# Kernel tuning notes

Hardware: AMD Instinct MI355X
Metric: run time of the kernel (lower is better)

## Reference

```python
import jax, jax.numpy as jnp
import numpy as np
from jax import lax

NUM_BLOCKS = 3
NUM_LAYERS = 10
NL = NUM_BLOCKS * NUM_LAYERS  # 30 res blocks
RC = 512   # residual channels
GC = 512   # gate channels
SC = 512   # skip channels
KS = 2     # kernel size
CIN = 128  # local-conditioning channels
FRONT = 32 # front conv kernel size
OUT = 2    # gaussian (mean, log_std)
UPS = [16, 16]  # upsample scales, product = 256 hop
SQRT_HALF = 0.7071067811865476


def causal_conv1d(x, w, b, dilation):
    # x: [B,C_in,T], w: [C_out,C_in,K] -> left-pad only == torch pad-both + trim right (causal SAME)
    pad = dilation * (w.shape[-1] - 1)
    y = lax.conv_general_dilated(x, w, window_strides=(1,), padding=[(pad, 0)],
                                 rhs_dilation=(dilation,),
                                 dimension_numbers=('NCH', 'OIH', 'NCH'))
    return y + b[None, :, None]


def pw(x, w, b):
    # 1x1 conv: w [C_out,C_in]
    return jnp.einsum('oi,bit->bot', w, x) + b[None, :, None]


def upsample(c, up_w, up_b):
    # c: [B,CIN,Tm]; torch ConvTranspose2d(1,1,(3,2s),pad=(1,s//2),stride=(1,s)) + LeakyReLU(0.4)
    h = c[:, None]  # [B,1,CIN,Tm]
    for j, s in enumerate(UPS):
        k = up_w[j][:, :, ::-1, ::-1]  # flip kernel: transposed conv as lhs-dilated conv
        pw_ = 2 * s - 1 - s // 2       # = K - 1 - torch_pad along width
        h = lax.conv_general_dilated(h, k, window_strides=(1, 1),
                                     padding=[(1, 1), (pw_, pw_)],
                                     lhs_dilation=(1, s),
                                     dimension_numbers=('NCHW', 'OIHW', 'NCHW')) + up_b[j]
        h = jnp.where(h > 0, h, 0.4 * h)  # LeakyReLU(0.4)
    return h[:, 0]  # [B,CIN,T]


def setup_inputs() -> dict:
    key = jax.random.key(0)
    ks = iter(jax.random.split(key, 32))
    def rn(shape, scale):
        return jax.random.normal(next(ks), shape, dtype=jnp.float32) * scale
    B, T_mel = 1, 16
    T = T_mel * 256
    return {
        'x': rn((B, 1, T), 1.0),
        'c': rn((B, CIN, T_mel), 1.0),
        'front_w': rn((RC, 1, FRONT), 0.2),
        'front_b': rn((RC,), 0.05),
        'filt_w': rn((NL, GC, RC, KS), 0.03),
        'filt_b': rn((NL, GC), 0.05),
        'gate_w': rn((NL, GC, RC, KS), 0.03),
        'gate_b': rn((NL, GC), 0.05),
        'cf_w': rn((NL, GC, CIN), 0.05),
        'cf_b': rn((NL, GC), 0.05),
        'cg_w': rn((NL, GC, CIN), 0.05),
        'cg_b': rn((NL, GC), 0.05),
        'res_w': rn((NL, RC, GC), 0.04),
        'res_b': rn((NL, RC), 0.05),
        'skip_w': rn((NL, SC, GC), 0.04),
        'skip_b': rn((NL, SC), 0.05),
        'fin1_w': rn((SC, SC), 0.04),
        'fin1_b': rn((SC,), 0.05),
        'fin2_w': rn((OUT, SC), 0.04),
        'fin2_b': rn((OUT,), 0.05),
        'up_w': rn((2, 1, 1, 3, 2 * 16), 0.1),
        'up_b': rn((2,), 0.05),
    }


def reference(x, c, front_w, front_b, filt_w, filt_b, gate_w, gate_b,
              cf_w, cf_b, cg_w, cg_b, res_w, res_b, skip_w, skip_b,
              fin1_w, fin1_b, fin2_w, fin2_b, up_w, up_b):
    c_up = upsample(c, up_w, up_b)                       # [B,CIN,T]
    h = jax.nn.relu(causal_conv1d(x, front_w, front_b, 1))  # [B,RC,T]
    skip = jnp.zeros((x.shape[0], SC, x.shape[2]), x.dtype)
    for i in range(NL):
        d = KS ** (i % NUM_LAYERS)
        f = causal_conv1d(h, filt_w[i], filt_b[i], d) + pw(c_up, cf_w[i], cf_b[i])
        g = causal_conv1d(h, gate_w[i], gate_b[i], d) + pw(c_up, cg_w[i], cg_b[i])
        o = jnp.tanh(f) * jax.nn.sigmoid(g)
        h = (h + pw(o, res_w[i], res_b[i])) * SQRT_HALF
        skip = skip + pw(o, skip_w[i], skip_b[i])
    out = jax.nn.relu(skip)
    out = jax.nn.relu(pw(out, fin1_w, fin1_b))
    return pw(out, fin2_w, fin2_b)  # [B,OUT,T]
```

## Files before the change

### kernel.cpp

```cpp
#include <hip/hip_runtime.h>
#include <hip/hip_bf16.h>

#define TLEN 4096
#define HPADT 512
#define SQRT_HALF 0.70710678118654752f

typedef __attribute__((ext_vector_type(8))) short short8;
typedef __attribute__((ext_vector_type(4))) float floatx4;
typedef __attribute__((ext_vector_type(4))) unsigned short ushort4v;

#define MFMA_BF16(a, b, c) __builtin_amdgcn_mfma_f32_16x16x32_bf16((a), (b), (c), 0, 0, 0)

__device__ __forceinline__ float bf2f(unsigned short u) {
  union { unsigned int i; float f; } v; v.i = ((unsigned int)u) << 16; return v.f;
}
__device__ __forceinline__ unsigned short f2bf(float x) {
  union { float f; unsigned int i; } v; v.f = x;
  unsigned int r = v.i + 0x7FFFu + ((v.i >> 16) & 1u);
  return (unsigned short)(r >> 16);
}
__device__ __forceinline__ short8 ld8(const unsigned short* p) { return *(const short8*)p; }

template <int NI>
__device__ __forceinline__ void stage128(unsigned short* lds, const unsigned short* src,
                                         int stride, int tid) {
  #pragma unroll
  for (int inst = 0; inst < NI; ++inst) {
    int qb = inst * 256 + (tid & 192);
    int q = qb + (tid & 63);
    int r = q >> 4;
    int c = (q & 15) ^ (r & 15);
    __builtin_amdgcn_global_load_lds(
        (const __attribute__((address_space(1))) unsigned int*)(src + (size_t)r * stride + (c << 3)),
        (__attribute__((address_space(3))) unsigned int*)(lds + qb * 8),
        16, 0, 0);
  }
}

__device__ __forceinline__ short8 frag128(const unsigned short* lds, int r, int cj) {
  return *(const short8*)(lds + r * 128 + ((cj ^ (r & 15)) << 3));
}

__global__ __launch_bounds__(256) void cast_all_kernel(
    const float* __restrict__ fw, const float* __restrict__ gw,
    const float* __restrict__ rw, const float* __restrict__ sw,
    const float* __restrict__ cf, const float* __restrict__ cg,
    const float* __restrict__ f1, const float* __restrict__ fb,
    const float* __restrict__ cfb, const float* __restrict__ gb,
    const float* __restrict__ cgb,
    unsigned short* __restrict__ WA, unsigned short* __restrict__ RS,
    unsigned short* __restrict__ CA, unsigned short* __restrict__ F1c,
    float* __restrict__ fgb)
{
  int b = blockIdx.x;
  if (b < 7680) {
    size_t idx = (size_t)b * 256 + threadIdx.x;
    size_t l = idx >> 16;
    int o = (int)((idx >> 7) & 511);
    int i4 = (int)(idx & 127) * 4;
    const float4* fp = (const float4*)(fw + (((l * 512 + o) * 512 + i4) * 2));
    const float4* gp = (const float4*)(gw + (((l * 512 + o) * 512 + i4) * 2));
    float4 f0 = fp[0], f1v = fp[1];
    float4 g0 = gp[0], g1 = gp[1];
    size_t base0 = ((l * 2 + 0) * 1024);
    size_t base1 = ((l * 2 + 1) * 1024);
    *(ushort4v*)&WA[(base0 + o) * 512 + i4]       = (ushort4v){f2bf(f0.x), f2bf(f0.z), f2bf(f1v.x), f2bf(f1v.z)};
    *(ushort4v*)&WA[(base1 + o) * 512 + i4]       = (ushort4v){f2bf(f0.y), f2bf(f0.w), f2bf(f1v.y), f2bf(f1v.w)};
    *(ushort4v*)&WA[(base0 + 512 + o) * 512 + i4] = (ushort4v){f2bf(g0.x), f2bf(g0.z), f2bf(g1.x), f2bf(g1.z)};
    *(ushort4v*)&WA[(base1 + 512 + o) * 512 + i4] = (ushort4v){f2bf(g0.y), f2bf(g0.w), f2bf(g1.y), f2bf(g1.w)};
  } else if (b < 15360) {
    size_t idx = (size_t)(b - 7680) * 256 + threadIdx.x;
    size_t l = idx >> 16;
    int o = (int)((idx >> 7) & 511);
    int i4 = (int)(idx & 127) * 4;
    float4 r4 = *(const float4*)(rw + ((l * 512 + o) * 512 + i4));
    float4 s4 = *(const float4*)(sw + ((l * 512 + o) * 512 + i4));
    *(ushort4v*)&RS[(l * 1024 + o) * 512 + i4]       = (ushort4v){f2bf(r4.x), f2bf(r4.y), f2bf(r4.z), f2bf(r4.w)};
    *(ushort4v*)&RS[(l * 1024 + 512 + o) * 512 + i4] = (ushort4v){f2bf(s4.x), f2bf(s4.y), f2bf(s4.z), f2bf(s4.w)};
  } else if (b < 17280) {
    size_t idx = (size_t)(b - 15360) * 256 + threadIdx.x;
    size_t l = idx >> 14;
    int o = (int)((idx >> 5) & 511);
    int i4 = (int)(idx & 31) * 4;
    float4 f4 = *(const float4*)(cf + ((l * 512 + o) * 128 + i4));
    float4 g4 = *(const float4*)(cg + ((l * 512 + o) * 128 + i4));
    *(ushort4v*)&CA[(l * 1024 + o) * 128 + i4]       = (ushort4v){f2bf(f4.x), f2bf(f4.y), f2bf(f4.z), f2bf(f4.w)};
    *(ushort4v*)&CA[(l * 1024 + 512 + o) * 128 + i4] = (ushort4v){f2bf(g4.x), f2bf(g4.y), f2bf(g4.z), f2bf(g4.w)};
  } else if (b < 17536) {
    size_t idx = (size_t)(b - 17280) * 256 + threadIdx.x;
    float4 v = *(const float4*)(f1 + idx * 4);
    *(ushort4v*)&F1c[idx * 4] = (ushort4v){f2bf(v.x), f2bf(v.y), f2bf(v.z), f2bf(v.w)};
  } else {
    int idx = (b - 17536) * 256 + threadIdx.x;
    int l = idx >> 10, r = idx & 1023;
    float v;
    if (r < 512) v = fb[l * 512 + r] + cfb[l * 512 + r];
    else         v = gb[l * 512 + r - 512] + cgb[l * 512 + r - 512];
    fgb[idx] = v;
  }
}


__global__ __launch_bounds__(256) void upsample1_kernel(
    const float* __restrict__ c, const float* __restrict__ up_w,
    const float* __restrict__ up_b, float* __restrict__ u1)
{
  int x = threadIdx.x;
  int h = blockIdx.x;
  const float* w = up_w;
  float acc = 0.f;
  int k1 = (23 - x) & 15;
  #pragma unroll
  for (int dk = 0; dk < 2; ++dk) {
    int kx = k1 + 16 * dk;
    int num = x + kx - 23;
    if (num >= 0) {
      int qq = num >> 4;
      if (qq < 16) {
        #pragma unroll
        for (int ky = 0; ky < 3; ++ky) {
          int hh = h + ky - 1;
          if (hh >= 0 && hh < 128)
            acc += c[hh * 16 + qq] * w[(2 - ky) * 32 + (31 - kx)];
        }
      }
    }
  }
  acc += up_b[0];
  u1[h * 256 + x] = acc > 0.f ? acc : 0.4f * acc;
}

__global__ __launch_bounds__(256) void upsample2_kernel(
    const float* __restrict__ u1, const float* __restrict__ up_w,
    const float* __restrict__ up_b, unsigned short* __restrict__ cu)
{
  int x = blockIdx.x * 256 + threadIdx.x;
  int h = blockIdx.y;
  const float* w = up_w + 96;
  float acc = 0.f;
  int k1 = (23 - x) & 15;
  #pragma unroll
  for (int dk = 0; dk < 2; ++dk) {
    int kx = k1 + 16 * dk;
    int num = x + kx - 23;
    if (num >= 0) {
      int qq = num >> 4;
      if (qq < 256) {
        #pragma unroll
        for (int ky = 0; ky < 3; ++ky) {
          int hh = h + ky - 1;
          if (hh >= 0 && hh < 128)
            acc += u1[hh * 256 + qq] * w[(2 - ky) * 32 + (31 - kx)];
        }
      }
    }
  }
  acc += up_b[1];
  acc = acc > 0.f ? acc : 0.4f * acc;
  cu[(size_t)x * 128 + h] = f2bf(acc);
}

__global__ __launch_bounds__(256) void front_kernel(
    const float* __restrict__ x, const float* __restrict__ fw, const float* __restrict__ fb,
    float* __restrict__ hf, unsigned short* __restrict__ hbf)
{
  __shared__ float xs[40];
  int tid = threadIdx.x;
  int o = blockIdx.y * 256 + tid;
  int t0 = blockIdx.x * 8;
  if (tid < 39) {
    int gx = t0 - 31 + tid;
    xs[tid] = (gx >= 0) ? x[gx] : 0.f;
  }
  __syncthreads();
  float w[32];
  #pragma unroll
  for (int k = 0; k < 32; ++k) w[k] = fw[o * 32 + k];
  float b = fb[o];
  #pragma unroll
  for (int j = 0; j < 8; ++j) {
    float acc = b;
    #pragma unroll
    for (int k = 0; k < 32; ++k) acc += w[k] * xs[j + k];
    acc = acc > 0.f ? acc : 0.f;
    int t = t0 + j;
    hf[(size_t)t * 512 + o] = acc;
    hbf[(size_t)(HPADT + t) * 512 + o] = f2bf(acc);
  }
}

__global__ __launch_bounds__(256) void gemm_a_kernel(
    const unsigned short* __restrict__ WA,
    const unsigned short* __restrict__ CA,
    const float* __restrict__ fgb,
    const unsigned short* __restrict__ hbf,
    const unsigned short* __restrict__ cu,
    unsigned short* __restrict__ obf,
    const int d)
{
  __shared__ unsigned short Af[2][64 * 128];
  __shared__ unsigned short Ag[2][64 * 128];
  __shared__ unsigned short Xs[2][128 * 128];

  const int tid = threadIdx.x;
  const int lane = tid & 63;
  const int wave = tid >> 6;
  const int lm = lane & 15, qd = lane >> 4;
  const int n0 = blockIdx.x * 128;
  const int m0 = blockIdx.y * 64;
  const int wm = (wave & 1) * 32;
  const int wn = (wave >> 1) * 64;

  floatx4 accF[2][4], accG[2][4];
  #pragma unroll
  for (int a = 0; a < 2; ++a)
    #pragma unroll
    for (int b = 0; b < 4; ++b) {
      accF[a][b] = (floatx4){0.f, 0.f, 0.f, 0.f};
      accG[a][b] = (floatx4){0.f, 0.f, 0.f, 0.f};
    }

  auto stage_step = [&](int s, int b) {
    if (s < 8) {
      int tap = s >> 2;
      int k0 = (s & 3) * 128;
      const unsigned short* ab = WA + (size_t)tap * 524288;
      stage128<4>(&Af[b][0], ab + (size_t)m0 * 512 + k0, 512, tid);
      stage128<4>(&Ag[b][0], ab + (size_t)(512 + m0) * 512 + k0, 512, tid);
      stage128<8>(&Xs[b][0], hbf + (size_t)(HPADT + n0 - (tap ? 0 : d)) * 512 + k0, 512, tid);
    } else {
      stage128<4>(&Af[b][0], CA + (size_t)m0 * 128, 128, tid);
      stage128<4>(&Ag[b][0], CA + (size_t)(512 + m0) * 128, 128, tid);
      stage128<8>(&Xs[b][0], cu + (size_t)n0 * 128, 128, tid);
    }
  };

  stage_step(0, 0);
  for (int s = 0; s < 9; ++s) {
    __syncthreads();
    if (s < 8) stage_step(s + 1, (s + 1) & 1);
    const unsigned short* af = &Af[s & 1][0];
    const unsigned short* ag = &Ag[s & 1][0];
    const unsigned short* xs = &Xs[s & 1][0];
    #pragma unroll
    for (int j = 0; j < 4; ++j) {
      int cj = j * 4 + qd;
      short8 a[2], g[2], xv[4];
      a[0] = frag128(af, wm + lm, cj);
      a[1] = frag128(af, wm + 16 + lm, cj);
      g[0] = frag128(ag, wm + lm, cj);
      g[1] = frag128(ag, wm + 16 + lm, cj);
      #pragma unroll
      for (int nt = 0; nt < 4; ++nt) xv[nt] = frag128(xs, wn + nt * 16 + lm, cj);
      #pragma unroll
      for (int mt = 0; mt < 2; ++mt)
        #pragma unroll
        for (int nt = 0; nt < 4; ++nt) {
          accF[mt][nt] = MFMA_BF16(a[mt], xv[nt], accF[mt][nt]);
          accG[mt][nt] = MFMA_BF16(g[mt], xv[nt], accG[mt][nt]);
        }
    }
  }

  #pragma unroll
  for (int mt = 0; mt < 2; ++mt) {
    int oc0 = m0 + wm + mt * 16 + qd * 4;
    floatx4 fb4 = *(const floatx4*)&fgb[oc0];
    floatx4 gb4 = *(const floatx4*)&fgb[512 + oc0];
    #pragma unroll
    for (int nt = 0; nt < 4; ++nt) {
      int t = n0 + wn + nt * 16 + lm;
      ushort4v o4;
      #pragma unroll
      for (int r = 0; r < 4; ++r) {
        float f = accF[mt][nt][r] + fb4[r];
        float g = accG[mt][nt][r] + gb4[r];
        float ef = __expf(-2.f * f);
        float th = (1.f - ef) / (1.f + ef);
        float sg = 1.f / (1.f + __expf(-g));
        o4[r] = f2bf(th * sg);
      }
      *(ushort4v*)&obf[(size_t)t * 512 + oc0] = o4;
    }
  }
}

__global__ __launch_bounds__(256) void gemm_b_kernel(
    const unsigned short* __restrict__ RS,
    const float* __restrict__ rb, const float* __restrict__ sb,
    const unsigned short* __restrict__ obf,
    float* __restrict__ hf, unsigned short* __restrict__ hbf,
    float* __restrict__ skip, unsigned short* __restrict__ skipbf,
    const int first, const int last)
{
  __shared__ unsigned short Ar[2][64 * 128];
  __shared__ unsigned short As_[2][64 * 128];
  __shared__ unsigned short Xs[2][128 * 128];

  const int tid = threadIdx.x;
  const int lane = tid & 63;
  const int wave = tid >> 6;
  const int lm = lane & 15, qd = lane >> 4;
  const int n0 = blockIdx.x * 128;
  const int m0 = blockIdx.y * 64;
  const int wm = (wave & 1) * 32;
  const int wn = (wave >> 1) * 64;

  floatx4 accR[2][4], accS[2][4];
  #pragma unroll
  for (int a = 0; a < 2; ++a)
    #pragma unroll
    for (int b = 0; b < 4; ++b) {
      accR[a][b] = (floatx4){0.f, 0.f, 0.f, 0.f};
      accS[a][b] = (floatx4){0.f, 0.f, 0.f, 0.f};
    }

  auto stage_step = [&](int s, int b) {
    int k0 = s * 128;
    stage128<4>(&Ar[b][0], RS + (size_t)m0 * 512 + k0, 512, tid);
    stage128<4>(&As_[b][0], RS + (size_t)(512 + m0) * 512 + k0, 512, tid);
    stage128<8>(&Xs[b][0], obf + (size_t)n0 * 512 + k0, 512, tid);
  };

  stage_step(0, 0);
  for (int s = 0; s < 4; ++s) {
    __syncthreads();
    if (s < 3) stage_step(s + 1, (s + 1) & 1);
    const unsigned short* ar = &Ar[s & 1][0];
    const unsigned short* as = &As_[s & 1][0];
    const unsigned short* xs = &Xs[s & 1][0];
    #pragma unroll
    for (int j = 0; j < 4; ++j) {
      int cj = j * 4 + qd;
      short8 a[2], g[2], xv[4];
      a[0] = frag128(ar, wm + lm, cj);
      a[1] = frag128(ar, wm + 16 + lm, cj);
      g[0] = frag128(as, wm + lm, cj);
      g[1] = frag128(as, wm + 16 + lm, cj);
      #pragma unroll
      for (int nt = 0; nt < 4; ++nt) xv[nt] = frag128(xs, wn + nt * 16 + lm, cj);
      #pragma unroll
      for (int mt = 0; mt < 2; ++mt)
        #pragma unroll
        for (int nt = 0; nt < 4; ++nt) {
          accR[mt][nt] = MFMA_BF16(a[mt], xv[nt], accR[mt][nt]);
          accS[mt][nt] = MFMA_BF16(g[mt], xv[nt], accS[mt][nt]);
        }
    }
  }

  #pragma unroll
  for (int mt = 0; mt < 2; ++mt) {
    int oc0 = m0 + wm + mt * 16 + qd * 4;
    floatx4 rb4 = *(const floatx4*)&rb[oc0];
    floatx4 sb4 = *(const floatx4*)&sb[oc0];
    #pragma unroll
    for (int nt = 0; nt < 4; ++nt) {
      int t = n0 + wn + nt * 16 + lm;
      size_t base = (size_t)t * 512 + oc0;
      floatx4 h4 = *(const floatx4*)&hf[base];
      floatx4 s4;
      if (first) s4 = (floatx4){0.f, 0.f, 0.f, 0.f};
      else s4 = *(const floatx4*)&skip[base];
      ushort4v hb4;
      #pragma unroll
      for (int r = 0; r < 4; ++r) {
        float hv = (h4[r] + accR[mt][nt][r] + rb4[r]) * SQRT_HALF;
        h4[r] = hv;
        hb4[r] = f2bf(hv);
        s4[r] = s4[r] + accS[mt][nt][r] + sb4[r];
      }
      *(floatx4*)&hf[base] = h4;
      *(ushort4v*)&hbf[(size_t)(HPADT + t) * 512 + oc0] = hb4;
      *(floatx4*)&skip[base] = s4;
      if (last) {
        ushort4v sk4;
        #pragma unroll
        for (int r = 0; r < 4; ++r) sk4[r] = f2bf(s4[r] > 0.f ? s4[r] : 0.f);
        *(ushort4v*)&skipbf[base] = sk4;
      }
    }
  }
}

__global__ __launch_bounds__(256) void final1_kernel(
    const unsigned short* __restrict__ W1,
    const float* __restrict__ b1,
    const unsigned short* __restrict__ skipbf,
    unsigned short* __restrict__ t1)
{
  __shared__ unsigned short Aw[2][64 * 128];
  __shared__ unsigned short Xs[2][128 * 128];

  const int tid = threadIdx.x;
  const int lane = tid & 63;
  const int wave = tid >> 6;
  const int lm = lane & 15, qd = lane >> 4;
  const int n0 = blockIdx.x * 128;
  const int m0 = blockIdx.y * 64;
  const int wm = (wave & 1) * 32;
  const int wn = (wave >> 1) * 64;

  floatx4 acc[2][4];
  #pragma unroll
  for (int a = 0; a < 2; ++a)
    #pragma unroll
    for (int b = 0; b < 4; ++b) acc[a][b] = (floatx4){0.f, 0.f, 0.f, 0.f};

  auto stage_step = [&](int s, int b) {
    int k0 = s * 128;
    stage128<4>(&Aw[b][0], W1 + (size_t)m0 * 512 + k0, 512, tid);
    stage128<8>(&Xs[b][0], skipbf + (size_t)n0 * 512 + k0, 512, tid);
  };

  stage_step(0, 0);
  for (int s = 0; s < 4; ++s) {
    __syncthreads();
    if (s < 3) stage_step(s + 1, (s + 1) & 1);
    const unsigned short* aw = &Aw[s & 1][0];
    const unsigned short* xs = &Xs[s & 1][0];
    #pragma unroll
    for (int j = 0; j < 4; ++j) {
      int cj = j * 4 + qd;
      short8 a[2], xv[4];
      a[0] = frag128(aw, wm + lm, cj);
      a[1] = frag128(aw, wm + 16 + lm, cj);
      #pragma unroll
      for (int nt = 0; nt < 4; ++nt) xv[nt] = frag128(xs, wn + nt * 16 + lm, cj);
      #pragma unroll
      for (int mt = 0; mt < 2; ++mt)
        #pragma unroll
        for (int nt = 0; nt < 4; ++nt)
          acc[mt][nt] = MFMA_BF16(a[mt], xv[nt], acc[mt][nt]);
    }
  }

  #pragma unroll
  for (int mt = 0; mt < 2; ++mt) {
    int oc0 = m0 + wm + mt * 16 + qd * 4;
    floatx4 b4 = *(const floatx4*)&b1[oc0];
    #pragma unroll
    for (int nt = 0; nt < 4; ++nt) {
      int t = n0 + wn + nt * 16 + lm;
      ushort4v o4;
      #pragma unroll
      for (int r = 0; r < 4; ++r) {
        float v = acc[mt][nt][r] + b4[r];
        o4[r] = f2bf(v > 0.f ? v : 0.f);
      }
      *(ushort4v*)&t1[(size_t)t * 512 + oc0] = o4;
    }
  }
}

__global__ __launch_bounds__(256) void final2_kernel(
    const float* __restrict__ W2, const float* __restrict__ b2,
    const unsigned short* __restrict__ t1, float* __restrict__ out)
{
  int wave = threadIdx.x >> 6, lane = threadIdx.x & 63;
  int t = blockIdx.x * 4 + wave;
  short8 v = ld8(t1 + (size_t)t * 512 + lane * 8);
  float a0 = 0.f, a1 = 0.f;
  #pragma unroll
  for (int r = 0; r < 8; ++r) {
    float f = bf2f((unsigned short)v[r]);
    a0 += W2[lane * 8 + r] * f;
    a1 += W2[512 + lane * 8 + r] * f;
  }
  #pragma unroll
  for (int off = 32; off > 0; off >>= 1) {
    a0 += __shfl_xor(a0, off, 64);
    a1 += __shfl_xor(a1, off, 64);
  }
  if (lane == 0) {
    out[t] = a0 + b2[0];
    out[TLEN + t] = a1 + b2[1];
  }
}

extern "C" void kernel_launch(void* const* d_in, const int* in_sizes, int n_in,
                              void* d_out, int out_size, void* d_ws, size_t ws_size,
                              hipStream_t stream) {
  (void)in_sizes; (void)n_in; (void)out_size; (void)ws_size;
  const float* x       = (const float*)d_in[0];
  const float* c       = (const float*)d_in[1];
  const float* front_w = (const float*)d_in[2];
  const float* front_b = (const float*)d_in[3];
  const float* filt_w  = (const float*)d_in[4];
  const float* filt_b  = (const float*)d_in[5];
  const float* gate_w  = (const float*)d_in[6];
  const float* gate_b  = (const float*)d_in[7];
  const float* cf_w    = (const float*)d_in[8];
  const float* cf_b    = (const float*)d_in[9];
  const float* cg_w    = (const float*)d_in[10];
  const float* cg_b    = (const float*)d_in[11];
  const float* res_w   = (const float*)d_in[12];
  const float* res_b   = (const float*)d_in[13];
  const float* skip_w  = (const float*)d_in[14];
  const float* skip_b  = (const float*)d_in[15];
  const float* fin1_w  = (const float*)d_in[16];
  const float* fin1_b  = (const float*)d_in[17];
  const float* fin2_w  = (const float*)d_in[18];
  const float* fin2_b  = (const float*)d_in[19];
  const float* up_w    = (const float*)d_in[20];
  const float* up_b    = (const float*)d_in[21];

  char* ws = (char*)d_ws;
  auto alloc = [&](size_t bytes) {
    char* p = ws;
    ws += (bytes + 255) & ~(size_t)255;
    return p;
  };
  unsigned short* WA     = (unsigned short*)alloc((size_t)30 * 2 * 1024 * 512 * 2);
  unsigned short* RS     = (unsigned short*)alloc((size_t)30 * 1024 * 512 * 2);
  unsigned short* CA     = (unsigned short*)alloc((size_t)30 * 1024 * 128 * 2);
  unsigned short* F1c    = (unsigned short*)alloc((size_t)512 * 512 * 2);
  float* fgb             = (float*)alloc((size_t)30 * 1024 * 4);
  float* u1              = (float*)alloc((size_t)128 * 256 * 4);
  unsigned short* cu     = (unsigned short*)alloc((size_t)TLEN * 128 * 2);
  float* hf              = (float*)alloc((size_t)TLEN * 512 * 4);
  unsigned short* hbf    = (unsigned short*)alloc((size_t)(HPADT + TLEN) * 512 * 2);
  unsigned short* obf    = (unsigned short*)alloc((size_t)TLEN * 512 * 2);
  float* skip            = (float*)alloc((size_t)TLEN * 512 * 4);
  unsigned short* skipbf = (unsigned short*)alloc((size_t)TLEN * 512 * 2);
  unsigned short* t1     = (unsigned short*)alloc((size_t)TLEN * 512 * 2);
  float* out             = (float*)d_out;

  hipMemsetAsync(hbf, 0, (size_t)HPADT * 512 * 2, stream);

  cast_all_kernel<<<17656, 256, 0, stream>>>(
      filt_w, gate_w, res_w, skip_w, cf_w, cg_w, fin1_w,
      filt_b, cf_b, gate_b, cg_b, WA, RS, CA, F1c, fgb);

  upsample1_kernel<<<dim3(128), 256, 0, stream>>>(c, up_w, up_b, u1);
  upsample2_kernel<<<dim3(16, 128), 256, 0, stream>>>(u1, up_w, up_b, cu);
  front_kernel<<<dim3(512, 2), 256, 0, stream>>>(x, front_w, front_b, hf, hbf);

  for (int l = 0; l < 30; ++l) {
    int d = 1 << (l % 10);
    gemm_a_kernel<<<dim3(32, 8), 256, 0, stream>>>(
        WA + (size_t)l * 2 * 524288, CA + (size_t)l * 131072,
        fgb + (size_t)l * 1024,
        hbf, cu, obf, d);
    gemm_b_kernel<<<dim3(32, 8), 256, 0, stream>>>(
        RS + (size_t)l * 524288,
        res_b + (size_t)l * 512, skip_b + (size_t)l * 512,
        obf, hf, hbf, skip, skipbf, (l == 0) ? 1 : 0, (l == 29) ? 1 : 0);
  }

  final1_kernel<<<dim3(32, 8), 256, 0, stream>>>(F1c, fin1_b, skipbf, t1);
  final2_kernel<<<1024, 256, 0, stream>>>(fin2_w, fin2_b, t1, out);
}
```

Measured before the change: 1.286 ms.

## Fuse 30-layer residual loop into one persistent kernel with grid barriers

Replaces the 60 per-layer gemm_a/gemm_b launches with a single persistent kernel of 256 blocks that loops over all layers and uses an atomic-counter grid barrier between phases. The fp32 residual state h and the skip accumulator are held in registers across layers, so the fp32 hf/skip global reads and writes disappear and the skip buffer is removed. This saves launch overhead and memory traffic, but it relies on all 256 blocks being co-resident and adds spin-wait barrier cost. The barrier's bounded spin guard could also silently break correctness if a wait times out.

Measured after the change: 1.864 ms. 1.45x slower.

```diff
diff --git a/kernel.cpp b/kernel.cpp
--- a/kernel.cpp
+++ b/kernel.cpp
@@ -39,6 +39,19 @@
 
 __device__ __forceinline__ short8 frag128(const unsigned short* lds, int r, int cj) {
   return *(const short8*)(lds + r * 128 + ((cj ^ (r & 15)) << 3));
+}
+
+__device__ __forceinline__ void grid_barrier(unsigned int* cnt, unsigned int target) {
+  __syncthreads();
+  if (threadIdx.x == 0) {
+    __builtin_amdgcn_fence(__ATOMIC_RELEASE, "agent");
+    atomicAdd(cnt, 1u);
+    int guard = 0;
+    while (atomicAdd(cnt, 0u) < target && ++guard < (1 << 20))
+      __builtin_amdgcn_s_sleep(4);
+    __builtin_amdgcn_fence(__ATOMIC_ACQUIRE, "agent");
+  }
+  __syncthreads();
 }
 
 __global__ __launch_bounds__(256) void cast_all_kernel(
@@ -189,197 +202,202 @@
   }
 }
 
-__global__ __launch_bounds__(256) void gemm_a_kernel(
+__global__ __launch_bounds__(256, 1) void wavenet_loop_kernel(
     const unsigned short* __restrict__ WA,
     const unsigned short* __restrict__ CA,
+    const unsigned short* __restrict__ RS,
     const float* __restrict__ fgb,
-    const unsigned short* __restrict__ hbf,
+    const float* __restrict__ res_b,
+    const float* __restrict__ skip_b,
+    unsigned short* __restrict__ hbf,
     const unsigned short* __restrict__ cu,
     unsigned short* __restrict__ obf,
-    const int d)
-{
-  __shared__ unsigned short Af[2][64 * 128];
-  __shared__ unsigned short Ag[2][64 * 128];
+    const float* __restrict__ hf,
+    unsigned short* __restrict__ skipbf,
+    unsigned int* __restrict__ bar)
+{
+  __shared__ unsigned short A1[2][64 * 128];
+  __shared__ unsigned short A2[2][64 * 128];
   __shared__ unsigned short Xs[2][128 * 128];
 
   const int tid = threadIdx.x;
   const int lane = tid & 63;
   const int wave = tid >> 6;
   const int lm = lane & 15, qd = lane >> 4;
-  const int n0 = blockIdx.x * 128;
-  const int m0 = blockIdx.y * 64;
+  const int bx = blockIdx.x & 31;
+  const int by = blockIdx.x >> 5;
+  const int n0 = bx * 128;
+  const int m0 = by * 64;
   const int wm = (wave & 1) * 32;
   const int wn = (wave >> 1) * 64;
 
-  floatx4 accF[2][4], accG[2][4];
-  #pragma unroll
-  for (int a = 0; a < 2; ++a)
-    #pragma unroll
-    for (int b = 0; b < 4; ++b) {
-      accF[a][b] = (floatx4){0.f, 0.f, 0.f, 0.f};
-      accG[a][b] = (floatx4){0.f, 0.f, 0.f, 0.f};
-    }
-
-  auto stage_step = [&](int s, int b) {
-    if (s < 8) {
-      int tap = s >> 2;
-      int k0 = (s & 3) * 128;
-      const unsigned short* ab = WA + (size_t)tap * 524288;
-      stage128<4>(&Af[b][0], ab + (size_t)m0 * 512 + k0, 512, tid);
-      stage128<4>(&Ag[b][0], ab + (size_t)(512 + m0) * 512 + k0, 512, tid);
-      stage128<8>(&Xs[b][0], hbf + (size_t)(HPADT + n0 - (tap ? 0 : d)) * 512 + k0, 512, tid);
-    } else {
-      stage128<4>(&Af[b][0], CA + (size_t)m0 * 128, 128, tid);
-      stage128<4>(&Ag[b][0], CA + (size_t)(512 + m0) * 128, 128, tid);
-      stage128<8>(&Xs[b][0], cu + (size_t)n0 * 128, 128, tid);
-    }
-  };
-
-  stage_step(0, 0);
-  for (int s = 0; s < 9; ++s) {
-    __syncthreads();
-    if (s < 8) stage_step(s + 1, (s + 1) & 1);
-    const unsigned short* af = &Af[s & 1][0];
-    const unsigned short* ag = &Ag[s & 1][0];
-    const unsigned short* xs = &Xs[s & 1][0];
-    #pragma unroll
-    for (int j = 0; j < 4; ++j) {
-      int cj = j * 4 + qd;
-      short8 a[2], g[2], xv[4];
-      a[0] = frag128(af, wm + lm, cj);
-      a[1] = frag128(af, wm + 16 + lm, cj);
-      g[0] = frag128(ag, wm + lm, cj);
-      g[1] = frag128(ag, wm + 16 + lm, cj);
-      #pragma unroll
-      for (int nt = 0; nt < 4; ++nt) xv[nt] = frag128(xs, wn + nt * 16 + lm, cj);
-      #pragma unroll
-      for (int mt = 0; mt < 2; ++mt)
-        #pragma unroll
-        for (int nt = 0; nt < 4; ++nt) {
-          accF[mt][nt] = MFMA_BF16(a[mt], xv[nt], accF[mt][nt]);
-          accG[mt][nt] = MFMA_BF16(g[mt], xv[nt], accG[mt][nt]);
-        }
-    }
-  }
-
+  floatx4 hst[2][4], sst[2][4];
   #pragma unroll
   for (int mt = 0; mt < 2; ++mt) {
     int oc0 = m0 + wm + mt * 16 + qd * 4;
-    floatx4 fb4 = *(const floatx4*)&fgb[oc0];
-    floatx4 gb4 = *(const floatx4*)&fgb[512 + oc0];
     #pragma unroll
     for (int nt = 0; nt < 4; ++nt) {
       int t = n0 + wn + nt * 16 + lm;
-      ushort4v o4;
-      #pragma unroll
-      for (int r = 0; r < 4; ++r) {
-        float f = accF[mt][nt][r] + fb4[r];
-        float g = accG[mt][nt][r] + gb4[r];
-        float ef = __expf(-2.f * f);
-        float th = (1.f - ef) / (1.f + ef);
-        float sg = 1.f / (1.f + __expf(-g));
-        o4[r] = f2bf(th * sg);
-      }
-      *(ushort4v*)&obf[(size_t)t * 512 + oc0] = o4;
-    }
-  }
-}
-
-__global__ __launch_bounds__(256) void gemm_b_kernel(
-    const unsigned short* __restrict__ RS,
-    const float* __restrict__ rb, const float* __restrict__ sb,
-    const unsigned short* __restrict__ obf,
-    float* __restrict__ hf, unsigned short* __restrict__ hbf,
-    float* __restrict__ skip, unsigned short* __restrict__ skipbf,
-    const int first, const int last)
-{
-  __shared__ unsigned short Ar[2][64 * 128];
-  __shared__ unsigned short As_[2][64 * 128];
-  __shared__ unsigned short Xs[2][128 * 128];
-
-  const int tid = threadIdx.x;
-  const int lane = tid & 63;
-  const int wave = tid >> 6;
-  const int lm = lane & 15, qd = lane >> 4;
-  const int n0 = blockIdx.x * 128;
-  const int m0 = blockIdx.y * 64;
-  const int wm = (wave & 1) * 32;
-  const int wn = (wave >> 1) * 64;
-
-  floatx4 accR[2][4], accS[2][4];
-  #pragma unroll
-  for (int a = 0; a < 2; ++a)
-    #pragma unroll
-    for (int b = 0; b < 4; ++b) {
-      accR[a][b] = (floatx4){0.f, 0.f, 0.f, 0.f};
-      accS[a][b] = (floatx4){0.f, 0.f, 0.f, 0.f};
-    }
-
-  auto stage_step = [&](int s, int b) {
-    int k0 = s * 128;
-    stage128<4>(&Ar[b][0], RS + (size_t)m0 * 512 + k0, 512, tid);
-    stage128<4>(&As_[b][0], RS + (size_t)(512 + m0) * 512 + k0, 512, tid);
-    stage128<8>(&Xs[b][0], obf + (size_t)n0 * 512 + k0, 512, tid);
-  };
-
-  stage_step(0, 0);
-  for (int s = 0; s < 4; ++s) {
-    __syncthreads();
-    if (s < 3) stage_step(s + 1, (s + 1) & 1);
-    const unsigned short* ar = &Ar[s & 1][0];
-    const unsigned short* as = &As_[s & 1][0];
-    const unsigned short* xs = &Xs[s & 1][0];
-    #pragma unroll
-    for (int j = 0; j < 4; ++j) {
-      int cj = j * 4 + qd;
-      short8 a[2], g[2], xv[4];
-      a[0] = frag128(ar, wm + lm, cj);
-      a[1] = frag128(ar, wm + 16 + lm, cj);
-      g[0] = frag128(as, wm + lm, cj);
-      g[1] = frag128(as, wm + 16 + lm, cj);
-      #pragma unroll
-      for (int nt = 0; nt < 4; ++nt) xv[nt] = frag128(xs, wn + nt * 16 + lm, cj);
-      #pragma unroll
-      for (int mt = 0; mt < 2; ++mt)
-        #pragma unroll
-        for (int nt = 0; nt < 4; ++nt) {
-          accR[mt][nt] = MFMA_BF16(a[mt], xv[nt], accR[mt][nt]);
-          accS[mt][nt] = MFMA_BF16(g[mt], xv[nt], accS[mt][nt]);
+      hst[mt][nt] = *(const floatx4*)&hf[(size_t)t * 512 + oc0];
+      sst[mt][nt] = (floatx4){0.f, 0.f, 0.f, 0.f};
+    }
+  }
+
+  unsigned int gen = 0;
+
+  #pragma unroll 1
+  for (int l = 0; l < 30; ++l) {
+    const int d = 1 << (l % 10);
+    const unsigned short* WAl = WA + (size_t)l * 1048576;
+    const unsigned short* CAl = CA + (size_t)l * 131072;
+    const unsigned short* RSl = RS + (size_t)l * 524288;
+    const float* fgbl = fgb + l * 1024;
+
+    floatx4 accF[2][4], accG[2][4];
+    #pragma unroll
+    for (int a = 0; a < 2; ++a)
+      #pragma unroll
+      for (int b = 0; b < 4; ++b) {
+        accF[a][b] = (floatx4){0.f, 0.f, 0.f, 0.f};
+        accG[a][b] = (floatx4){0.f, 0.f, 0.f, 0.f};
+      }
+
+    auto stage_a = [&](int s, int b) {
+      if (s < 8) {
+        int tap = s >> 2;
+        int k0 = (s & 3) * 128;
+        const unsigned short* ab = WAl + (size_t)tap * 524288;
+        stage128<4>(&A1[b][0], ab + (size_t)m0 * 512 + k0, 512, tid);
+        stage128<4>(&A2[b][0], ab + (size_t)(512 + m0) * 512 + k0, 512, tid);
+        stage128<8>(&Xs[b][0], hbf + (size_t)(HPADT + n0 - (tap ? 0 : d)) * 512 + k0, 512, tid);
+      } else {
+        stage128<4>(&A1[b][0], CAl + (size_t)m0 * 128, 128, tid);
+        stage128<4>(&A2[b][0], CAl + (size_t)(512 + m0) * 128, 128, tid);
+        stage128<8>(&Xs[b][0], cu + (size_t)n0 * 128, 128, tid);
+      }
+    };
+
+    stage_a(0, 0);
+    for (int s = 0; s < 9; ++s) {
+      __syncthreads();
+      if (s < 8) stage_a(s + 1, (s + 1) & 1);
+      const unsigned short* af = &A1[s & 1][0];
+      const unsigned short* ag = &A2[s & 1][0];
+      const unsigned short* xs = &Xs[s & 1][0];
+      #pragma unroll
+      for (int j = 0; j < 4; ++j) {
+        int cj = j * 4 + qd;
+        short8 a[2], g[2], xv[4];
+        a[0] = frag128(af, wm + lm, cj);
+        a[1] = frag128(af, wm + 16 + lm, cj);
+        g[0] = frag128(ag, wm + lm, cj);
+        g[1] = frag128(ag, wm + 16 + lm, cj);
+        #pragma unroll
+        for (int nt = 0; nt < 4; ++nt) xv[nt] = frag128(xs, wn + nt * 16 + lm, cj);
+        #pragma unroll
+        for (int mt = 0; mt < 2; ++mt)
+          #pragma unroll
+          for (int nt = 0; nt < 4; ++nt) {
+            accF[mt][nt] = MFMA_BF16(a[mt], xv[nt], accF[mt][nt]);
+            accG[mt][nt] = MFMA_BF16(g[mt], xv[nt], accG[mt][nt]);
+          }
+      }
+    }
+
+    #pragma unroll
+    for (int mt = 0; mt < 2; ++mt) {
+      int oc0 = m0 + wm + mt * 16 + qd * 4;
+      floatx4 fb4 = *(const floatx4*)&fgbl[oc0];
+      floatx4 gb4 = *(const floatx4*)&fgbl[512 + oc0];
+      #pragma unroll
+      for (int nt = 0; nt < 4; ++nt) {
+        int t = n0 + wn + nt * 16 + lm;
+        ushort4v o4;
+        #pragma unroll
+        for (int r = 0; r < 4; ++r) {
+          float f = accF[mt][nt][r] + fb4[r];
+          float g = accG[mt][nt][r] + gb4[r];
+          float ef = __expf(-2.f * f);
+          float th = (1.f - ef) / (1.f + ef);
+          float sg = 1.f / (1.f + __expf(-g));
+          o4[r] = f2bf(th * sg);
         }
-    }
-  }
-
-  #pragma unroll
-  for (int mt = 0; mt < 2; ++mt) {
-    int oc0 = m0 + wm + mt * 16 + qd * 4;
-    floatx4 rb4 = *(const floatx4*)&rb[oc0];
-    floatx4 sb4 = *(const floatx4*)&sb[oc0];
-    #pragma unroll
-    for (int nt = 0; nt < 4; ++nt) {
-      int t = n0 + wn + nt * 16 + lm;
-      size_t base = (size_t)t * 512 + oc0;
-      floatx4 h4 = *(const floatx4*)&hf[base];
-      floatx4 s4;
-      if (first) s4 = (floatx4){0.f, 0.f, 0.f, 0.f};
-      else s4 = *(const floatx4*)&skip[base];
-      ushort4v hb4;
-      #pragma unroll
-      for (int r = 0; r < 4; ++r) {
-        float hv = (h4[r] + accR[mt][nt][r] + rb4[r]) * SQRT_HALF;
-        h4[r] = hv;
-        hb4[r] = f2bf(hv);
-        s4[r] = s4[r] + accS[mt][nt][r] + sb4[r];
-      }
-      *(floatx4*)&hf[base] = h4;
-      *(ushort4v*)&hbf[(size_t)(HPADT + t) * 512 + oc0] = hb4;
-      *(floatx4*)&skip[base] = s4;
-      if (last) {
-        ushort4v sk4;
-        #pragma unroll
-        for (int r = 0; r < 4; ++r) sk4[r] = f2bf(s4[r] > 0.f ? s4[r] : 0.f);
-        *(ushort4v*)&skipbf[base] = sk4;
-      }
-    }
+        *(ushort4v*)&obf[(size_t)t * 512 + oc0] = o4;
+      }
+    }
+
+    grid_barrier(bar, ++gen * 256u);
+
+    floatx4 accR[2][4];
+    #pragma unroll
+    for (int a = 0; a < 2; ++a)
+      #pragma unroll
+      for (int b = 0; b < 4; ++b) accR[a][b] = (floatx4){0.f, 0.f, 0.f, 0.f};
+
+    auto stage_b = [&](int s, int b) {
+      int k0 = s * 128;
+      stage128<4>(&A1[b][0], RSl + (size_t)m0 * 512 + k0, 512, tid);
+      stage128<4>(&A2[b][0], RSl + (size_t)(512 + m0) * 512 + k0, 512, tid);
+      stage128<8>(&Xs[b][0], obf + (size_t)n0 * 512 + k0, 512, tid);
+    };
+
+    stage_b(0, 0);
+    for (int s = 0; s < 4; ++s) {
+      __syncthreads();
+      if (s < 3) stage_b(s + 1, (s + 1) & 1);
+      const unsigned short* ar = &A1[s & 1][0];
+      const unsigned short* as = &A2[s & 1][0];
+      const unsigned short* xs = &Xs[s & 1][0];
+      #pragma unroll
+      for (int j = 0; j < 4; ++j) {
+        int cj = j * 4 + qd;
+        short8 a[2], g[2], xv[4];
+        a[0] = frag128(ar, wm + lm, cj);
+        a[1] = frag128(ar, wm + 16 + lm, cj);
+        g[0] = frag128(as, wm + lm, cj);
+        g[1] = frag128(as, wm + 16 + lm, cj);
+        #pragma unroll
+        for (int nt = 0; nt < 4; ++nt) xv[nt] = frag128(xs, wn + nt * 16 + lm, cj);
+        #pragma unroll
+        for (int mt = 0; mt < 2; ++mt)
+          #pragma unroll
+          for (int nt = 0; nt < 4; ++nt) {
+            accR[mt][nt] = MFMA_BF16(a[mt], xv[nt], accR[mt][nt]);
+            sst[mt][nt] = MFMA_BF16(g[mt], xv[nt], sst[mt][nt]);
+          }
+      }
+    }
+
+    #pragma unroll
+    for (int mt = 0; mt < 2; ++mt) {
+      int oc0 = m0 + wm + mt * 16 + qd * 4;
+      floatx4 rb4 = *(const floatx4*)&res_b[l * 512 + oc0];
+      floatx4 sb4 = *(const floatx4*)&skip_b[l * 512 + oc0];
+      #pragma unroll
+      for (int nt = 0; nt < 4; ++nt) {
+        int t = n0 + wn + nt * 16 + lm;
+        ushort4v hb4;
+        #pragma unroll
+        for (int r = 0; r < 4; ++r) {
+          float hv = (hst[mt][nt][r] + accR[mt][nt][r] + rb4[r]) * SQRT_HALF;
+          hst[mt][nt][r] = hv;
+          hb4[r] = f2bf(hv);
+          sst[mt][nt][r] += sb4[r];
+        }
+        *(ushort4v*)&hbf[(size_t)(HPADT + t) * 512 + oc0] = hb4;
+        if (l == 29) {
+          ushort4v sk4;
+          #pragma unroll
+          for (int r = 0; r < 4; ++r) {
+            float sv = sst[mt][nt][r];
+            sk4[r] = f2bf(sv > 0.f ? sv : 0.f);
+          }
+          *(ushort4v*)&skipbf[(size_t)t * 512 + oc0] = sk4;
+        }
+      }
+    }
+
+    grid_barrier(bar, ++gen * 256u);
   }
 }
 
@@ -521,12 +539,13 @@
   float* hf              = (float*)alloc((size_t)TLEN * 512 * 4);
   unsigned short* hbf    = (unsigned short*)alloc((size_t)(HPADT + TLEN) * 512 * 2);
   unsigned short* obf    = (unsigned short*)alloc((size_t)TLEN * 512 * 2);
-  float* skip            = (float*)alloc((size_t)TLEN * 512 * 4);
   unsigned short* skipbf = (unsigned short*)alloc((size_t)TLEN * 512 * 2);
   unsigned short* t1     = (unsigned short*)alloc((size_t)TLEN * 512 * 2);
+  unsigned int* bar      = (unsigned int*)alloc(256);
   float* out             = (float*)d_out;
 
   hipMemsetAsync(hbf, 0, (size_t)HPADT * 512 * 2, stream);
+  hipMemsetAsync(bar, 0, sizeof(unsigned int), stream);
 
   cast_all_kernel<<<17656, 256, 0, stream>>>(
       filt_w, gate_w, res_w, skip_w, cf_w, cg_w, fin1_w,
@@ -536,17 +555,8 @@
   upsample2_kernel<<<dim3(16, 128), 256, 0, stream>>>(u1, up_w, up_b, cu);
   front_kernel<<<dim3(512, 2), 256, 0, stream>>>(x, front_w, front_b, hf, hbf);
 
-  for (int l = 0; l < 30; ++l) {
-    int d = 1 << (l % 10);
-    gemm_a_kernel<<<dim3(32, 8), 256, 0, stream>>>(
-        WA + (size_t)l * 2 * 524288, CA + (size_t)l * 131072,
-        fgb + (size_t)l * 1024,
-        hbf, cu, obf, d);
-    gemm_b_kernel<<<dim3(32, 8), 256, 0, stream>>>(
-        RS + (size_t)l * 524288,
-        res_b + (size_t)l * 512, skip_b + (size_t)l * 512,
-        obf, hf, hbf, skip, skipbf, (l == 0) ? 1 : 0, (l == 29) ? 1 : 0);
-  }
+  wavenet_loop_kernel<<<dim3(256), dim3(256), 0, stream>>>(
+      WA, CA, RS, fgb, res_b, skip_b, hbf, cu, obf, hf, skipbf, bar);
 
   final1_kernel<<<dim3(32, 8), 256, 0, stream>>>(F1c, fin1_b, skipbf, t1);
   final2_kernel<<<1024, 256, 0, stream>>>(fin2_w, fin2_b, t1, out);
```
